# Optimization experiments

Measured on AMD Instinct MI355X. Metric: run time of the kernel, lower is better.

## Reference

```python
import jax, jax.numpy as jnp
import numpy as np

N = 20000      # nodes
E1 = 100000    # topo (2d) edges
E2 = 100000    # distance edges
HID = 128      # hidden_size
N2D = 128      # node_embed_size_2d
E2D = 64       # edge_embed_size_2d
EF = 128       # edge_feat_size
ET = 32        # edge_type_size
NRBF = 64
CUT = 6.0


def rbf_expand(d):
    # Gaussian radial basis with cosine cutoff envelope, d: [E]
    centers = jnp.linspace(0.0, CUT, NRBF)
    width = CUT / NRBF
    env = 0.5 * (jnp.cos(jnp.pi * jnp.clip(d / CUT, 0.0, 1.0)) + 1.0)
    return jnp.exp(-((d[:, None] - centers) ** 2) / (2.0 * width * width)) * env[:, None]


def setup_inputs() -> dict:
    key = jax.random.key(0)
    ks = jax.random.split(key, 20)
    s = 0.02
    return {
        "H": jax.random.normal(ks[0], (N, HID), jnp.float32),
        "V": jax.random.normal(ks[1], (N, HID, 3), jnp.float32),
        "Z": jax.random.normal(ks[2], (N, 3), jnp.float32) * 3.0,
        "layer_i": 0,
        "H_2d": jax.random.normal(ks[3], (N, N2D), jnp.float32),
        "mask_2d": jnp.ones((N,), bool),
        "E2d_idx": jax.random.randint(ks[4], (2, E1), 0, N),
        "E2d_feat": jax.random.normal(ks[5], (E2D, E1), jnp.float32),
        "Z_3d": jax.random.normal(ks[6], (N, 3), jnp.float32) * 3.0,
        "mask_3d": jnp.ones((N,), bool),
        "Edist_idx": jax.random.randint(ks[7], (2, E2), 0, N),
        "Edist_val": jax.random.uniform(ks[8], (E2,), jnp.float32) * CUT,
        "virtual_node_embed": jax.random.normal(ks[9], (1, N2D), jnp.float32),
        "edge_type_embed": jax.random.normal(ks[10], (3, ET), jnp.float32),
        "W_rbf": jax.random.normal(ks[11], (EF, NRBF), jnp.float32) * s,
        "W_e2d": jax.random.normal(ks[12], (EF, E2D), jnp.float32) * s,
        "W_i": jax.random.normal(ks[13], (HID, HID + N2D), jnp.float32) * s,
        "W_phi1": jax.random.normal(ks[14], (HID, HID + EF + ET), jnp.float32) * s,
        "b_phi1": jnp.zeros((HID,), jnp.float32),
        "W_phi2": jax.random.normal(ks[15], (3 * HID, HID), jnp.float32) * s,
        "b_phi2": jnp.zeros((3 * HID,), jnp.float32),
        "W_msg": jax.random.normal(ks[16], (3 * HID, NRBF), jnp.float32) * s,
        "b_msg": jnp.zeros((3 * HID,), jnp.float32),
    }


def reference(H, V, Z, layer_i, H_2d, mask_2d, E2d_idx, E2d_feat, Z_3d, mask_3d,
              Edist_idx, Edist_val, virtual_node_embed, edge_type_embed,
              W_rbf, W_e2d, W_i, W_phi1, b_phi1, W_phi2, b_phi2, W_msg, b_msg):
    n = H.shape[0]
    # mask_3d is all-True in this fixture => n_cond_3d == n (static shapes)
    nodes_real = jnp.concatenate([H, H_2d], axis=-1)                       # [n, h1+h2]
    virt = jnp.broadcast_to(virtual_node_embed, (n, virtual_node_embed.shape[1]))
    nodes_virt = jnp.concatenate([H, virt], axis=-1)                        # [n, h1+h2]
    nodes = jnp.concatenate([nodes_real, nodes_virt], axis=0) @ W_i.T      # [2n, h1]
    v = jnp.concatenate([V, jnp.zeros_like(V)], axis=0)                     # [2n, h1, 3]
    z = jnp.concatenate([Z, Z_3d], axis=0)                                  # [2n, 3]

    row_3d = jnp.arange(n)
    col_3d = jnp.arange(n) + n
    E3d = jnp.stack([jnp.concatenate([row_3d, col_3d]),
                     jnp.concatenate([col_3d, row_3d])], axis=0)            # [2, 2n]
    edges = jnp.concatenate([E2d_idx, E3d, Edist_idx], axis=-1)             # [2, E]
    e1, e3, e2 = E2d_idx.shape[1], E3d.shape[1], Edist_idx.shape[1]
    edge_type = jnp.concatenate([jnp.zeros((e1,), jnp.int32),
                                 jnp.ones((e3,), jnp.int32),
                                 jnp.full((e2,), 2, jnp.int32)])
    et = edge_type_embed[edge_type]                                         # [E, ET]
    attr2d = E2d_feat.T @ W_e2d.T                                           # [e1, EF]
    attr3d = jnp.zeros((e3, W_e2d.shape[0]), jnp.float32)                   # [e3, EF]
    attrd = rbf_expand(Edist_val) @ W_rbf.T                                 # [e2, EF]
    edge_attr = jnp.concatenate(
        [jnp.concatenate([attr2d, attr3d, attrd], axis=0), et], axis=-1)    # [E, EF+ET]

    # AdapterLayer: PaiNN-style equivariant message passing
    row, col = edges[0], edges[1]
    rel = z[row] - z[col]                                                   # [E, 3]
    dist = jnp.sqrt(jnp.sum(rel * rel, axis=-1) + 1e-8)                     # [E]
    unit = rel / dist[:, None]
    phi_in = jnp.concatenate([nodes[col], edge_attr], axis=-1)
    phi = jax.nn.silu(phi_in @ W_phi1.T + b_phi1) @ W_phi2.T + b_phi2       # [E, 3h]
    wd = rbf_expand(dist) @ W_msg.T + b_msg                                 # [E, 3h]
    m = phi * wd
    h = nodes.shape[1]
    s_msg, v_gate, r_gate = m[:, :h], m[:, h:2 * h], m[:, 2 * h:]
    dv = v[col] * v_gate[:, :, None] + unit[:, None, :] * r_gate[:, :, None]  # [E, h, 3]
    nn2 = nodes.shape[0]
    H_add = jax.ops.segment_sum(s_msg, row, num_segments=nn2)[:n]
    V_add = jax.ops.segment_sum(dv, row, num_segments=nn2)[:n]

    # eval-mode clamp
    H_add = jnp.clip(H_add, -100.0, 100.0)
    V_add = jnp.clip(V_add, -100.0, 100.0)

    mask_dist = jnp.zeros((n,), bool).at[Edist_idx[0]].set(True).at[Edist_idx[1]].set(True)
    update_mask = mask_2d | mask_3d | mask_dist
    H_add = jnp.where(update_mask[:, None], H_add, 0.0)
    V_add = jnp.where(update_mask[:, None, None], V_add, 0.0)
    return H_add, V_add
```

## Files before the change

kernel.cpp:

```cpp
#include <hip/hip_runtime.h>
#include <hip/hip_bf16.h>

#define NN   20000
#define E1N  100000
#define E2N  100000
#define NEFF 220000
#define TILE 64
#define NBLK ((NEFF + TILE - 1) / TILE)
#define NPAD (NBLK * TILE)
#define RBF_STEP   0.09523809523809523f
#define RBF_INV2W2 56.88888888888889f

typedef short  bf16x8 __attribute__((ext_vector_type(8)));
typedef float  f32x4  __attribute__((ext_vector_type(4)));

__device__ __forceinline__ float4 ld4(const float* p) {
    return *reinterpret_cast<const float4*>(p);
}
__device__ __forceinline__ ushort f2bf(float x) {
    __hip_bfloat16 h = __float2bfloat16(x);
    return *reinterpret_cast<ushort*>(&h);
}
__device__ __forceinline__ float bf2f(ushort u) {
    return __uint_as_float(((unsigned)u) << 16);
}
__device__ __forceinline__ float env_of(float d) {
    float x = fminf(fmaxf(d * (1.0f / 6.0f), 0.0f), 1.0f);
    return 0.5f * (__cosf(3.14159265358979f * x) + 1.0f);
}

__device__ __forceinline__ int edge_row(int eid, const int* __restrict__ E2d_idx,
                                        const int* __restrict__ Edist_idx) {
    if (eid < E1N) return E2d_idx[eid];
    if (eid < E1N + NN) return eid - E1N;
    return Edist_idx[eid - E1N - NN];
}

__global__ __launch_bounds__(256) void hist_kernel(
    const int* __restrict__ E2d_idx, const int* __restrict__ Edist_idx,
    int* __restrict__ hist) {
    int g = blockIdx.x * 256 + threadIdx.x;
    if (g < NEFF) atomicAdd(&hist[edge_row(g, E2d_idx, Edist_idx)], 1);
}

__global__ __launch_bounds__(1024) void scan_kernel(
    const int* __restrict__ hist, int* __restrict__ start, int* __restrict__ cursor) {
    __shared__ int buf[1024];
    __shared__ int carry;
    const int t = threadIdx.x;
    if (t == 0) carry = 0;
    __syncthreads();
    for (int chunk = 0; chunk < 20; ++chunk) {
        int idx = chunk * 1024 + t;
        int v = (idx < NN) ? hist[idx] : 0;
        buf[t] = v;
        __syncthreads();
        for (int off = 1; off < 1024; off <<= 1) {
            int x = (t >= off) ? buf[t - off] : 0;
            __syncthreads();
            buf[t] += x;
            __syncthreads();
        }
        int excl  = buf[t] - v;
        int cbase = carry;
        int tot   = buf[1023];
        if (idx <= NN) {
            start[idx] = cbase + excl;
            if (idx < NN) cursor[idx] = cbase + excl;
        }
        __syncthreads();
        if (t == 0) carry = cbase + tot;
        __syncthreads();
    }
}

__global__ __launch_bounds__(256) void scatter_kernel(
    const int* __restrict__ E2d_idx, const int* __restrict__ Edist_idx,
    int* __restrict__ cursor, int* __restrict__ order) {
    int g = blockIdx.x * 256 + threadIdx.x;
    if (g < NEFF) {
        int r = edge_row(g, E2d_idx, Edist_idx);
        int pos = atomicAdd(&cursor[r], 1);
        order[pos] = g;
    }
}

__global__ __launch_bounds__(64) void chunkrow_kernel(
    const int* __restrict__ order, const int* __restrict__ E2d_idx,
    const int* __restrict__ Edist_idx, int cap, int nch, int* __restrict__ chunk_r0) {
    int i = threadIdx.x;
    if (i < nch) {
        int p = i * cap;
        if (p >= NEFF) p = NEFF - 1;
        chunk_r0[i] = edge_row(order[p], E2d_idx, Edist_idx);
    }
}

__global__ __launch_bounds__(256) void meta_kernel(
    const int* __restrict__ order, const int* __restrict__ E2d_idx,
    const int* __restrict__ Edist_idx, const float* __restrict__ Edist_val,
    const float* __restrict__ Z, const float* __restrict__ Z3d,
    int4* __restrict__ metaI, float4* __restrict__ metaF,
    float4* __restrict__ payloadU) {
    int g = blockIdx.x * 256 + threadIdx.x;
    if (g >= NPAD) return;
    int eid = (g < NEFF) ? order[g] : -1;
    int row, col, ty, e2 = 0; float dval = 0.f;
    if (eid < 0)             { ty = 1; row = -1; col = 0; }
    else if (eid < E1N)      { ty = 0; row = E2d_idx[eid]; col = E2d_idx[E1N + eid]; e2 = eid; }
    else if (eid < E1N + NN) { ty = 1; int jj = eid - E1N; row = jj; col = jj + NN; }
    else { ty = 2; int g2 = eid - E1N - NN;
           row = Edist_idx[g2]; col = Edist_idx[E2N + g2]; dval = Edist_val[g2]; }
    int rs = (row < 0) ? 0 : row;
    float prx = Z[rs * 3], pry = Z[rs * 3 + 1], prz = Z[rs * 3 + 2];
    float pcx, pcy, pcz;
    if (col < NN) { pcx = Z[col * 3]; pcy = Z[col * 3 + 1]; pcz = Z[col * 3 + 2]; }
    else { int c = col - NN; pcx = Z3d[c * 3]; pcy = Z3d[c * 3 + 1]; pcz = Z3d[c * 3 + 2]; }
    float dx = prx - pcx, dy = pry - pcy, dz = prz - pcz;
    float dist = sqrtf(dx * dx + dy * dy + dz * dz + 1e-8f);
    float inv = 1.0f / dist;
    int vcol = (col < NN) ? col : -1;
    metaI[g] = make_int4(col, row, ty, e2);
    metaF[g] = make_float4(dist, dval, env_of(dist), env_of(dval));
    if (row >= 0)
        payloadU[g] = make_float4(dx * inv, dy * inv, dz * inv, __int_as_float(vcol));
}

__global__ __launch_bounds__(256) void prep_kernel(
    const float* __restrict__ W_phi1, const float* __restrict__ b_phi1,
    const float* __restrict__ W_e2d, const float* __restrict__ W_rbf,
    const float* __restrict__ W_phi2, const float* __restrict__ W_msg,
    const float* __restrict__ et, const float* __restrict__ W_i,
    ushort* __restrict__ W1c, ushort* __restrict__ W2b,
    ushort* __restrict__ Wmb, float* __restrict__ b_type,
    ushort* __restrict__ Wib) {
    int g = blockIdx.x * 256 + threadIdx.x;
    if (g < 32768) {
        int n = g >> 8, k = g & 255;
        float v;
        if (k < 128) v = W_phi1[n * 288 + k];
        else {
            int kk = k - 128;
            const float* Wsel = (kk < 64) ? W_e2d : W_rbf;
            int j = kk & 63;
            float s = 0.f;
            for (int a = 0; a < 128; ++a) s += W_phi1[n * 288 + 128 + a] * Wsel[a * 64 + j];
            v = s;
        }
        W1c[n * 256 + k] = f2bf(v);
    } else if (g < 81920) {
        int q = g - 32768; W2b[q] = f2bf(W_phi2[q]);
    } else if (g < 106496) {
        int q = g - 81920; Wmb[q] = f2bf(W_msg[q]);
    } else if (g < 106880) {
        int q = g - 106496; int ty = q >> 7, n = q & 127;
        float s = b_phi1[n];
        for (int a = 0; a < 32; ++a) s += W_phi1[n * 288 + 256 + a] * et[ty * 32 + a];
        b_type[q] = s;
    } else if (g < 139648) {
        int q = g - 106880; Wib[q] = f2bf(W_i[q]);
    }
}

__global__ __launch_bounds__(256) void featT_kernel(
    const float* __restrict__ feat, ushort* __restrict__ featTb) {
    __shared__ float tile[64][65];
    const int t = threadIdx.x;
    const int cbase = blockIdx.x * 64;
    for (int i = t; i < 64 * 64; i += 256) {
        int k = i >> 6, e = i & 63;
        tile[k][e] = (cbase + e < E1N) ? feat[(size_t)k * E1N + cbase + e] : 0.f;
    }
    __syncthreads();
    for (int i = t; i < 64 * 64; i += 256) {
        int e = i >> 6, k = i & 63;
        if (cbase + e < E1N) featTb[(size_t)(cbase + e) * 64 + k] = f2bf(tile[k][e]);
    }
}

__global__ __launch_bounds__(256, 2) void nodes_mfma_kernel(
    const float* __restrict__ H, const float* __restrict__ H2d,
    const float* __restrict__ virt, const ushort* __restrict__ Wib,
    ushort* __restrict__ nodesb) {
    __shared__ ushort A[64][264];
    __shared__ ushort WB[128][132];

    const int t = threadIdx.x;
    const int gbase = blockIdx.x * 64;

    for (int i = t; i < 64 * 64; i += 256) {
        int e = i >> 6, q = i & 63;
        int row = gbase + e;
        float4 v;
        if (q < 32)          v = ld4(H + (size_t)((row < NN) ? row : row - NN) * 128 + q * 4);
        else if (row < NN)   v = ld4(H2d + (size_t)row * 128 + (q - 32) * 4);
        else                 v = ld4(virt + (q - 32) * 4);
        ushort tmp[4] = {f2bf(v.x), f2bf(v.y), f2bf(v.z), f2bf(v.w)};
        *reinterpret_cast<uint2*>(&A[e][q * 4]) = *reinterpret_cast<const uint2*>(tmp);
    }
    for (int i = t; i < 128 * 16; i += 256) {
        int n = i >> 4, q = i & 15;
        *reinterpret_cast<uint4*>(&WB[n][q * 8]) =
            *reinterpret_cast<const uint4*>(Wib + (size_t)n * 256 + q * 8);
    }
    __syncthreads();

    const int w  = t >> 6, lane = t & 63;
    const int mh = w >> 1, nh = w & 1;
    const int lr = lane >> 4, lc = lane & 15;
    const int ar0 = mh * 32 + lc;

    f32x4 acc[2][4];
#pragma unroll
    for (int mt = 0; mt < 2; ++mt)
#pragma unroll
        for (int nt = 0; nt < 4; ++nt) acc[mt][nt] = (f32x4){0.f, 0.f, 0.f, 0.f};
#pragma unroll
    for (int ks = 0; ks < 4; ++ks) {
        bf16x8 a0 = *reinterpret_cast<const bf16x8*>(&A[ar0][ks * 32 + lr * 8]);
        bf16x8 a1 = *reinterpret_cast<const bf16x8*>(&A[ar0 + 16][ks * 32 + lr * 8]);
#pragma unroll
        for (int nt = 0; nt < 4; ++nt) {
            int n = nh * 64 + nt * 16 + lc;
            bf16x8 b = *reinterpret_cast<const bf16x8*>(&WB[n][ks * 32 + lr * 8]);
            acc[0][nt] = __builtin_amdgcn_mfma_f32_16x16x32_bf16(a0, b, acc[0][nt], 0, 0, 0);
            acc[1][nt] = __builtin_amdgcn_mfma_f32_16x16x32_bf16(a1, b, acc[1][nt], 0, 0, 0);
        }
    }
    __syncthreads();
    for (int i = t; i < 128 * 16; i += 256) {
        int n = i >> 4, q = i & 15;
        *reinterpret_cast<uint4*>(&WB[n][q * 8]) =
            *reinterpret_cast<const uint4*>(Wib + (size_t)n * 256 + 128 + q * 8);
    }
    __syncthreads();
#pragma unroll
    for (int ks = 4; ks < 8; ++ks) {
        bf16x8 a0 = *reinterpret_cast<const bf16x8*>(&A[ar0][ks * 32 + lr * 8]);
        bf16x8 a1 = *reinterpret_cast<const bf16x8*>(&A[ar0 + 16][ks * 32 + lr * 8]);
#pragma unroll
        for (int nt = 0; nt < 4; ++nt) {
            int n = nh * 64 + nt * 16 + lc;
            bf16x8 b = *reinterpret_cast<const bf16x8*>(&WB[n][(ks - 4) * 32 + lr * 8]);
            acc[0][nt] = __builtin_amdgcn_mfma_f32_16x16x32_bf16(a0, b, acc[0][nt], 0, 0, 0);
            acc[1][nt] = __builtin_amdgcn_mfma_f32_16x16x32_bf16(a1, b, acc[1][nt], 0, 0, 0);
        }
    }
#pragma unroll
    for (int mt = 0; mt < 2; ++mt)
#pragma unroll
        for (int nt = 0; nt < 4; ++nt)
#pragma unroll
            for (int r = 0; r < 4; ++r) {
                int e  = mh * 32 + mt * 16 + lr * 4 + r;
                int ch = nh * 64 + nt * 16 + lc;
                nodesb[(size_t)(gbase + e) * 128 + ch] = f2bf(acc[mt][nt][r]);
            }
}

template <int MODE>
__global__ __launch_bounds__(256, 2) void edge_kernel(
    const ushort* __restrict__ nodesb, const float* __restrict__ V,
    const float* __restrict__ Z, const float* __restrict__ Z3d,
    const int* __restrict__ E2d_idx, const float* __restrict__ E2d_feat,
    const ushort* __restrict__ featTb,
    const int* __restrict__ Edist_idx, const float* __restrict__ Edist_val,
    const ushort* __restrict__ W1c, const ushort* __restrict__ W2b,
    const ushort* __restrict__ Wmb, const float* __restrict__ b_type,
    const float* __restrict__ b_phi2, const float* __restrict__ b_msg,
    const int4* __restrict__ metaI, const float4* __restrict__ metaF,
    int p0, ushort* __restrict__ payloadM,
    float* __restrict__ Hout, float* __restrict__ Vout) {

    __shared__ ushort A1f[TILE * 264 + 256];
    __shared__ ushort WB[128][132];
    __shared__ float  s_bt[3][128];
    __shared__ int    s_row[TILE], s_col[TILE], s_ty[TILE], s_e2[TILE], s_vcol[TILE];
    __shared__ float  s_dist[TILE], s_dval[TILE], s_env[TILE], s_env2[TILE];
    __shared__ float  s_unit[TILE][3];

    ushort* hidp  = A1f;
    ushort* m_lds = A1f + 8704;

    const int t = threadIdx.x;
    const int gbase = blockIdx.x * TILE;

    if (MODE == 1) {
        if (t < TILE) {
            int4 mi = metaI[p0 + gbase + t];
            s_col[t] = mi.x; s_row[t] = mi.y; s_ty[t] = mi.z; s_e2[t] = mi.w;
        } else if (t < 2 * TILE) {
            int e = t - TILE;
            float4 mf = metaF[p0 + gbase + e];
            s_dist[e] = mf.x; s_dval[e] = mf.y; s_env[e] = mf.z; s_env2[e] = mf.w;
        }
    } else {
        if (t < TILE) {
            int gpos = gbase + t;
            int eid = (gpos < NEFF) ? gpos : -1;
            int row, col, ty, e2 = 0; float dval = 0.f;
            if (eid < 0)             { ty = 1; row = -1; col = 0; }
            else if (eid < E1N)      { ty = 0; row = E2d_idx[eid]; col = E2d_idx[E1N + eid]; e2 = eid; }
            else if (eid < E1N + NN) { ty = 1; int jj = eid - E1N; row = jj; col = jj + NN; }
            else { ty = 2; int g2 = eid - E1N - NN;
                   row = Edist_idx[g2]; col = Edist_idx[E2N + g2]; dval = Edist_val[g2]; }
            int rs = (row < 0) ? 0 : row;
            float prx = Z[rs * 3], pry = Z[rs * 3 + 1], prz = Z[rs * 3 + 2];
            float pcx, pcy, pcz;
            if (col < NN) { pcx = Z[col * 3]; pcy = Z[col * 3 + 1]; pcz = Z[col * 3 + 2]; }
            else { int c = col - NN; pcx = Z3d[c * 3]; pcy = Z3d[c * 3 + 1]; pcz = Z3d[c * 3 + 2]; }
            float dx = prx - pcx, dy = pry - pcy, dz = prz - pcz;
            float dist = sqrtf(dx * dx + dy * dy + dz * dz + 1e-8f);
            float inv = 1.0f / dist;
            s_row[t] = row; s_col[t] = col; s_ty[t] = ty; s_e2[t] = e2;
            s_vcol[t] = (col < NN) ? col : -1;
            s_unit[t][0] = dx * inv; s_unit[t][1] = dy * inv; s_unit[t][2] = dz * inv;
            s_dist[t] = dist; s_dval[t] = dval;
            s_env[t] = env_of(dist); s_env2[t] = env_of(dval);
        }
    }
    for (int i = t; i < 384; i += 256) ((float*)s_bt)[i] = b_type[i];
    __syncthreads();

    for (int i = t; i < TILE * 16; i += 256) {
        int e = i >> 4, q = i & 15;
        *reinterpret_cast<uint4*>(&A1f[e * 264 + q * 8]) =
            *reinterpret_cast<const uint4*>(nodesb + (size_t)s_col[e] * 128 + q * 8);
    }
    if (MODE == 1) {
        for (int i = t; i < TILE * 128; i += 256) {
            int e = i >> 7, k = i & 127;
            int ty = s_ty[e];
            ushort v = 0;
            if (ty == 0) { if (k < 64) v = featTb[(size_t)s_e2[e] * 64 + k]; }
            else if (ty == 2) {
                if (k >= 64) {
                    float dd = s_dval[e] - (float)(k - 64) * RBF_STEP;
                    v = f2bf(__expf(-dd * dd * RBF_INV2W2) * s_env2[e]);
                }
            }
            A1f[e * 264 + 128 + k] = v;
        }
    } else {
        for (int i = t; i < TILE * 128; i += 256) {
            int k = i >> 6, e = i & 63;
            int ty = s_ty[e];
            float v = 0.f;
            if (ty == 0) { if (k < 64) v = E2d_feat[(size_t)k * E1N + s_e2[e]]; }
            else if (ty == 2) {
                if (k >= 64) {
                    float dd = s_dval[e] - (float)(k - 64) * RBF_STEP;
                    v = __expf(-dd * dd * RBF_INV2W2) * s_env2[e];
                }
            }
            A1f[e * 264 + 128 + k] = f2bf(v);
        }
    }
    for (int i = t; i < 128 * 16; i += 256) {
        int n = i >> 4, q = i & 15;
        *reinterpret_cast<uint4*>(&WB[n][q * 8]) =
            *reinterpret_cast<const uint4*>(W1c + (size_t)n * 256 + q * 8);
    }
    __syncthreads();

    const int w  = t >> 6, lane = t & 63;
    const int mh = w >> 1, nh = w & 1;
    const int lr = lane >> 4, lc = lane & 15;
    const int ar0 = mh * 32 + lc;

    bf16x8 ra0[2], ra1[2];
    {
        float dA = s_dist[ar0],      eA = s_env[ar0];
        float dB = s_dist[ar0 + 16], eB = s_env[ar0 + 16];
#pragma unroll
        for (int ks = 0; ks < 2; ++ks)
#pragma unroll
            for (int j = 0; j < 8; ++j) {
                float c  = (float)(ks * 32 + lr * 8 + j) * RBF_STEP;
                float tA = dA - c, tB = dB - c;
                ra0[ks][j] = (short)f2bf(__expf(-tA * tA * RBF_INV2W2) * eA);
                ra1[ks][j] = (short)f2bf(__expf(-tB * tB * RBF_INV2W2) * eB);
            }
    }

    f32x4 acc[2][4];
#pragma unroll
    for (int mt = 0; mt < 2; ++mt)
#pragma unroll
        for (int nt = 0; nt < 4; ++nt) acc[mt][nt] = (f32x4){0.f, 0.f, 0.f, 0.f};
#pragma unroll
    for (int ks = 0; ks < 4; ++ks) {
        bf16x8 a0 = *reinterpret_cast<const bf16x8*>(&A1f[ar0 * 264 + ks * 32 + lr * 8]);
        bf16x8 a1 = *reinterpret_cast<const bf16x8*>(&A1f[(ar0 + 16) * 264 + ks * 32 + lr * 8]);
#pragma unroll
        for (int nt = 0; nt < 4; ++nt) {
            int n = nh * 64 + nt * 16 + lc;
            bf16x8 b = *reinterpret_cast<const bf16x8*>(&WB[n][ks * 32 + lr * 8]);
            acc[0][nt] = __builtin_amdgcn_mfma_f32_16x16x32_bf16(a0, b, acc[0][nt], 0, 0, 0);
            acc[1][nt] = __builtin_amdgcn_mfma_f32_16x16x32_bf16(a1, b, acc[1][nt], 0, 0, 0);
        }
    }
    __syncthreads();
    for (int i = t; i < 128 * 16; i += 256) {
        int n = i >> 4, q = i & 15;
        *reinterpret_cast<uint4*>(&WB[n][q * 8]) =
            *reinterpret_cast<const uint4*>(W1c + (size_t)n * 256 + 128 + q * 8);
    }
    __syncthreads();
#pragma unroll
    for (int ks = 4; ks < 8; ++ks) {
        bf16x8 a0 = *reinterpret_cast<const bf16x8*>(&A1f[ar0 * 264 + ks * 32 + lr * 8]);
        bf16x8 a1 = *reinterpret_cast<const bf16x8*>(&A1f[(ar0 + 16) * 264 + ks * 32 + lr * 8]);
#pragma unroll
        for (int nt = 0; nt < 4; ++nt) {
            int n = nh * 64 + nt * 16 + lc;
            bf16x8 b = *reinterpret_cast<const bf16x8*>(&WB[n][(ks - 4) * 32 + lr * 8]);
            acc[0][nt] = __builtin_amdgcn_mfma_f32_16x16x32_bf16(a0, b, acc[0][nt], 0, 0, 0);
            acc[1][nt] = __builtin_amdgcn_mfma_f32_16x16x32_bf16(a1, b, acc[1][nt], 0, 0, 0);
        }
    }
    __syncthreads();

#pragma unroll
    for (int mt = 0; mt < 2; ++mt)
#pragma unroll
        for (int nt = 0; nt < 4; ++nt)
#pragma unroll
            for (int r = 0; r < 4; ++r) {
                int e  = mh * 32 + mt * 16 + lr * 4 + r;
                int ch = nh * 64 + nt * 16 + lc;
                float x = acc[mt][nt][r] + s_bt[s_ty[e]][ch];
                hidp[e * 136 + ch] = f2bf(x / (1.0f + __expf(-x)));
            }
    for (int i = t; i < 128 * 16; i += 256) {
        int n = i >> 4, q = i & 15;
        *reinterpret_cast<uint4*>(&WB[n][q * 8]) =
            *reinterpret_cast<const uint4*>(W2b + (size_t)n * 128 + q * 8);
    }
    __syncthreads();

    bf16x8 ha0[4], ha1[4];
#pragma unroll
    for (int ks = 0; ks < 4; ++ks) {
        ha0[ks] = *reinterpret_cast<const bf16x8*>(&hidp[ar0 * 136 + ks * 32 + lr * 8]);
        ha1[ks] = *reinterpret_cast<const bf16x8*>(&hidp[(ar0 + 16) * 136 + ks * 32 + lr * 8]);
    }

    f32x4 vgr[2][4];
#pragma unroll
    for (int c = 0; c < 3; ++c) {
        f32x4 p[2][4], g[2][4];
#pragma unroll
        for (int mt = 0; mt < 2; ++mt)
#pragma unroll
            for (int nt = 0; nt < 4; ++nt) {
                p[mt][nt] = (f32x4){0.f, 0.f, 0.f, 0.f};
                g[mt][nt] = (f32x4){0.f, 0.f, 0.f, 0.f};
            }
#pragma unroll
        for (int ks = 0; ks < 4; ++ks) {
#pragma unroll
            for (int nt = 0; nt < 4; ++nt) {
                int n = nh * 64 + nt * 16 + lc;
                bf16x8 b = *reinterpret_cast<const bf16x8*>(&WB[n][ks * 32 + lr * 8]);
                p[0][nt] = __builtin_amdgcn_mfma_f32_16x16x32_bf16(ha0[ks], b, p[0][nt], 0, 0, 0);
                p[1][nt] = __builtin_amdgcn_mfma_f32_16x16x32_bf16(ha1[ks], b, p[1][nt], 0, 0, 0);
            }
        }
#pragma unroll
        for (int ks = 0; ks < 2; ++ks) {
#pragma unroll
            for (int nt = 0; nt < 4; ++nt) {
                int n = c * 128 + nh * 64 + nt * 16 + lc;
                bf16x8 b = *reinterpret_cast<const bf16x8*>(Wmb + (size_t)n * 64 + ks * 32 + lr * 8);
                g[0][nt] = __builtin_amdgcn_mfma_f32_16x16x32_bf16(ra0[ks], b, g[0][nt], 0, 0, 0);
                g[1][nt] = __builtin_amdgcn_mfma_f32_16x16x32_bf16(ra1[ks], b, g[1][nt], 0, 0, 0);
            }
        }
        __syncthreads();
        if (c < 2) {
            for (int i = t; i < 128 * 16; i += 256) {
                int n = i >> 4, q = i & 15;
                *reinterpret_cast<uint4*>(&WB[n][q * 8]) =
                    *reinterpret_cast<const uint4*>(W2b + (size_t)((c + 1) * 128 + n) * 128 + q * 8);
            }
        }
#pragma unroll
        for (int mt = 0; mt < 2; ++mt)
#pragma unroll
            for (int nt = 0; nt < 4; ++nt) {
                int d  = nh * 64 + nt * 16 + lc;
                float b2 = b_phi2[c * 128 + d];
                float bm = b_msg[c * 128 + d];
#pragma unroll
                for (int r = 0; r < 4; ++r) {
                    int e = mh * 32 + mt * 16 + lr * 4 + r;
                    float m = (p[mt][nt][r] + b2) * (g[mt][nt][r] + bm);
                    if (MODE == 1) {
                        m_lds[e * 132 + d] = f2bf(m);
                    } else {
                        int row = s_row[e];
                        if (c == 0) {
                            if (row >= 0) unsafeAtomicAdd(&Hout[(size_t)row * 128 + d], m);
                        } else if (c == 1) {
                            vgr[mt][nt][r] = m;
                        } else if (row >= 0) {
                            float vgv = vgr[mt][nt][r];
                            int vc = s_vcol[e];
                            float vx = 0.f, vy = 0.f, vz = 0.f;
                            if (vc >= 0) {
                                const float* vp = V + ((size_t)vc * 128 + d) * 3;
                                vx = vp[0]; vy = vp[1]; vz = vp[2];
                            }
                            float* vo = Vout + ((size_t)row * 128 + d) * 3;
                            unsafeAtomicAdd(vo + 0, vx * vgv + s_unit[e][0] * m);
                            unsafeAtomicAdd(vo + 1, vy * vgv + s_unit[e][1] * m);
                            unsafeAtomicAdd(vo + 2, vz * vgv + s_unit[e][2] * m);
                        }
                    }
                }
            }
        __syncthreads();
        if (MODE == 1) {
            for (int i = t; i < 2048; i += 256) {
                int e = i >> 5, q = i & 31;
                *reinterpret_cast<uint2*>(payloadM + (size_t)(gbase + e) * 384 + c * 128 + q * 4) =
                    *reinterpret_cast<const uint2*>(m_lds + e * 132 + q * 4);
            }
        }
    }
}

__global__ __launch_bounds__(256) void reduce_kernel(
    const ushort* __restrict__ payloadM, const float4* __restrict__ payloadU,
    const float* __restrict__ V, const int* __restrict__ start,
    const int* __restrict__ chunk_r0, int ci, int p0, int p1,
    float* __restrict__ Hout, float* __restrict__ Vout) {
    const int t = threadIdx.x;
    const int rbase = chunk_r0[ci] + blockIdx.x * 8;
    const bool hside = (t < 128);
    const int d = hside ? t : (t - 128);
    for (int nr = 0; nr < 8; ++nr) {
        int r = rbase + nr;
        if (r >= NN) return;
        int s0 = start[r], s1 = start[r + 1];
        if (s0 >= p1) return;
        int a = (s0 > p0) ? s0 : p0;
        int b = (s1 < p1) ? s1 : p1;
        if (a >= b) continue;
        int n = b - a;
        if (hside) {
            const ushort* base = payloadM + (size_t)(a - p0) * 384 + d;
            float a0 = 0.f, a1 = 0.f, a2 = 0.f, a3 = 0.f;
            int i = 0;
            for (; i + 4 <= n; i += 4) {
                a0 += bf2f(base[(size_t)i * 384]);
                a1 += bf2f(base[(size_t)(i + 1) * 384]);
                a2 += bf2f(base[(size_t)(i + 2) * 384]);
                a3 += bf2f(base[(size_t)(i + 3) * 384]);
            }
            for (; i < n; ++i) a0 += bf2f(base[(size_t)i * 384]);
            float acc = (a0 + a1) + (a2 + a3);
            float* ptr = &Hout[(size_t)r * 128 + d];
            float o = *ptr + acc;
            if (s1 <= p1) o = fminf(fmaxf(o, -100.f), 100.f);
            *ptr = o;
        } else {
            const ushort* base = payloadM + (size_t)(a - p0) * 384;
            const float4* ub = payloadU + a;
            float ax = 0.f, ay = 0.f, az = 0.f;
            float bx = 0.f, by = 0.f, bz = 0.f;
            int i = 0;
            for (; i + 2 <= n; i += 2) {
                const ushort* pm0 = base + (size_t)i * 384;
                const ushort* pm1 = base + (size_t)(i + 1) * 384;
                float vg0 = bf2f(pm0[128 + d]), rg0 = bf2f(pm0[256 + d]);
                float vg1 = bf2f(pm1[128 + d]), rg1 = bf2f(pm1[256 + d]);
                float4 u0 = ub[i];
                float4 u1 = ub[i + 1];
                int vc0 = __float_as_int(u0.w);
                int vc1 = __float_as_int(u1.w);
                if (vc0 >= 0) {
                    const float* vp = V + (size_t)vc0 * 384 + d * 3;
                    ax += vg0 * vp[0]; ay += vg0 * vp[1]; az += vg0 * vp[2];
                }
                if (vc1 >= 0) {
                    const float* vp = V + (size_t)vc1 * 384 + d * 3;
                    bx += vg1 * vp[0]; by += vg1 * vp[1]; bz += vg1 * vp[2];
                }
                ax += rg0 * u0.x; ay += rg0 * u0.y; az += rg0 * u0.z;
                bx += rg1 * u1.x; by += rg1 * u1.y; bz += rg1 * u1.z;
            }
            if (i < n) {
                const ushort* pm0 = base + (size_t)i * 384;
                float vg0 = bf2f(pm0[128 + d]), rg0 = bf2f(pm0[256 + d]);
                float4 u0 = ub[i];
                int vc0 = __float_as_int(u0.w);
                if (vc0 >= 0) {
                    const float* vp = V + (size_t)vc0 * 384 + d * 3;
                    ax += vg0 * vp[0]; ay += vg0 * vp[1]; az += vg0 * vp[2];
                }
                ax += rg0 * u0.x; ay += rg0 * u0.y; az += rg0 * u0.z;
            }
            ax += bx; ay += by; az += bz;
            float* vo = Vout + (size_t)r * 384 + d * 3;
            float ox = vo[0] + ax, oy = vo[1] + ay, oz = vo[2] + az;
            if (s1 <= p1) {
                ox = fminf(fmaxf(ox, -100.f), 100.f);
                oy = fminf(fmaxf(oy, -100.f), 100.f);
                oz = fminf(fmaxf(oz, -100.f), 100.f);
            }
            vo[0] = ox; vo[1] = oy; vo[2] = oz;
        }
    }
}

extern "C" void kernel_launch(void* const* d_in, const int* in_sizes, int n_in,
                              void* d_out, int out_size, void* d_ws, size_t ws_size,
                              hipStream_t stream) {
    const float* H         = (const float*)d_in[0];
    const float* V         = (const float*)d_in[1];
    const float* Z         = (const float*)d_in[2];
    const float* H2d       = (const float*)d_in[4];
    const int*   E2d_idx   = (const int*)d_in[6];
    const float* E2d_feat  = (const float*)d_in[7];
    const float* Z3d       = (const float*)d_in[8];
    const int*   Edist_idx = (const int*)d_in[10];
    const float* Edist_val = (const float*)d_in[11];
    const float* virt      = (const float*)d_in[12];
    const float* et        = (const float*)d_in[13];
    const float* W_rbf     = (const float*)d_in[14];
    const float* W_e2d     = (const float*)d_in[15];
    const float* W_i       = (const float*)d_in[16];
    const float* W_phi1    = (const float*)d_in[17];
    const float* b_phi1    = (const float*)d_in[18];
    const float* W_phi2    = (const float*)d_in[19];
    const float* b_phi2    = (const float*)d_in[20];
    const float* W_msg     = (const float*)d_in[21];
    const float* b_msg     = (const float*)d_in[22];

    ushort* nodesb  = (ushort*)d_ws;
    ushort* W1c     = nodesb + 5120000;
    ushort* W2b     = W1c + 32768;
    ushort* Wmb     = W2b + 49152;
    ushort* Wib     = Wmb + 24576;
    float*  b_type  = (float*)(Wib + 32768);
    ushort* featTb  = (ushort*)(b_type + 384);
    int*    hist    = (int*)(featTb + (size_t)E1N * 64);
    int*    cursor  = hist + NN;
    int*    start   = cursor + NN;
    int*    order   = start + NN + 1;
    int*    chunk_r0= order + NPAD;
    int4*   metaI   = (int4*)(((size_t)(chunk_r0 + 64) + 15) & ~(size_t)15);
    float4* metaF   = (float4*)(metaI + NPAD);
    float4* payloadU= metaF + NPAD;

    size_t fixed = (size_t)((char*)(payloadU + NPAD) - (char*)d_ws);
    size_t poff  = (fixed + 255) & ~(size_t)255;
    size_t avail = (ws_size > poff) ? (ws_size - poff) : 0;
    long long cap_ll = (long long)(avail / 768) / TILE * TILE;
    int cap = (cap_ll > (long long)NPAD) ? NPAD : (int)cap_ll;
    const bool big = (cap >= 4096);
    ushort* payloadM = (ushort*)((char*)d_ws + poff);

    float* Hout = (float*)d_out;
    float* Vout = Hout + (size_t)NN * 128;

    hipMemsetAsync(d_out, 0, (size_t)out_size * sizeof(float), stream);
    prep_kernel<<<(139648 + 255) / 256, 256, 0, stream>>>(
        W_phi1, b_phi1, W_e2d, W_rbf, W_phi2, W_msg, et, W_i,
        W1c, W2b, Wmb, b_type, Wib);
    nodes_mfma_kernel<<<(2 * NN) / 64, 256, 0, stream>>>(H, H2d, virt, Wib, nodesb);

    if (big) {
        hipMemsetAsync(hist, 0, NN * sizeof(int), stream);
        featT_kernel<<<(E1N + 63) / 64, 256, 0, stream>>>(E2d_feat, featTb);
        hist_kernel<<<(NEFF + 255) / 256, 256, 0, stream>>>(E2d_idx, Edist_idx, hist);
        scan_kernel<<<1, 1024, 0, stream>>>(hist, start, cursor);
        scatter_kernel<<<(NEFF + 255) / 256, 256, 0, stream>>>(E2d_idx, Edist_idx, cursor, order);
        meta_kernel<<<(NPAD + 255) / 256, 256, 0, stream>>>(
            order, E2d_idx, Edist_idx, Edist_val, Z, Z3d, metaI, metaF, payloadU);
        int bpc = cap / TILE;
        int nch = (NBLK + bpc - 1) / bpc;
        chunkrow_kernel<<<1, 64, 0, stream>>>(order, E2d_idx, Edist_idx, cap, nch, chunk_r0);
        int rbound = (NN < cap + 1) ? NN : (cap + 1);
        int rgrid  = (rbound + 7) / 8;
        for (int ci = 0; ci < nch; ++ci) {
            int b0 = ci * bpc;
            int nb = ((NBLK - b0) < bpc) ? (NBLK - b0) : bpc;
            int p0 = b0 * TILE;
            int p1 = p0 + nb * TILE; if (p1 > NEFF) p1 = NEFF;
            edge_kernel<1><<<nb, 256, 0, stream>>>(
                nodesb, V, Z, Z3d, E2d_idx, E2d_feat, featTb, Edist_idx, Edist_val,
                W1c, W2b, Wmb, b_type, b_phi2, b_msg, metaI, metaF, p0, payloadM,
                Hout, Vout);
            reduce_kernel<<<rgrid, 256, 0, stream>>>(payloadM, payloadU, V, start,
                                                     chunk_r0, ci, p0, p1, Hout, Vout);
        }
    } else {
        edge_kernel<0><<<NBLK, 256, 0, stream>>>(
            nodesb, V, Z, Z3d, E2d_idx, E2d_feat, featTb, Edist_idx, Edist_val,
            W1c, W2b, Wmb, b_type, b_phi2, b_msg, metaI, metaF, 0, payloadM,
            Hout, Vout);
    }
}
```

Measured before the change: 405.2 us.

## Single-pass edge kernel with register A-operands and unchunked CSR reduce

Replaces the chunked edge/reduce loop with one edge kernel over all edges followed by one reduce pass, provided the workspace can hold the whole bf16 message payload. The reduce now writes clipped results directly, so the output memset, the chunk-row kernel and the read-modify-write of outputs are all dropped. The new edge kernel builds its A operands in registers straight from global memory instead of staging them in LDS, which shrinks shared memory enough to allow 3 blocks per CU. The scan is rewritten as a 256-thread serial-plus-shuffle scan. The trade-offs are a large workspace requirement and possibly higher register pressure at the new occupancy target.

Result: slower. 443.7 us (+9.5%).

```diff
diff --git a/kernel.cpp b/kernel.cpp
--- a/kernel.cpp
+++ b/kernel.cpp
@@ -28,6 +28,9 @@
     float x = fminf(fmaxf(d * (1.0f / 6.0f), 0.0f), 1.0f);
     return 0.5f * (__cosf(3.14159265358979f * x) + 1.0f);
 }
+__device__ __forceinline__ float clip100(float x) {
+    return fminf(fmaxf(x, -100.f), 100.f);
+}
 
 __device__ __forceinline__ int edge_row(int eid, const int* __restrict__ E2d_idx,
                                         const int* __restrict__ Edist_idx) {
@@ -43,35 +46,36 @@
     if (g < NEFF) atomicAdd(&hist[edge_row(g, E2d_idx, Edist_idx)], 1);
 }
 
-__global__ __launch_bounds__(1024) void scan_kernel(
+__global__ __launch_bounds__(256) void scan_kernel(
     const int* __restrict__ hist, int* __restrict__ start, int* __restrict__ cursor) {
-    __shared__ int buf[1024];
-    __shared__ int carry;
+    __shared__ int wsum[4];
     const int t = threadIdx.x;
-    if (t == 0) carry = 0;
-    __syncthreads();
-    for (int chunk = 0; chunk < 20; ++chunk) {
-        int idx = chunk * 1024 + t;
-        int v = (idx < NN) ? hist[idx] : 0;
-        buf[t] = v;
-        __syncthreads();
-        for (int off = 1; off < 1024; off <<= 1) {
-            int x = (t >= off) ? buf[t - off] : 0;
-            __syncthreads();
-            buf[t] += x;
-            __syncthreads();
-        }
-        int excl  = buf[t] - v;
-        int cbase = carry;
-        int tot   = buf[1023];
-        if (idx <= NN) {
-            start[idx] = cbase + excl;
-            if (idx < NN) cursor[idx] = cbase + excl;
-        }
-        __syncthreads();
-        if (t == 0) carry = cbase + tot;
-        __syncthreads();
-    }
+    const int base = t * 80;
+    int s = 0;
+    for (int j = 0; j < 80; ++j) {
+        int idx = base + j;
+        if (idx < NN) s += hist[idx];
+    }
+    const int lane = t & 63, w = t >> 6;
+    int v = s;
+    for (int off = 1; off < 64; off <<= 1) {
+        int x = __shfl_up(v, off, 64);
+        if (lane >= off) v += x;
+    }
+    if (lane == 63) wsum[w] = v;
+    __syncthreads();
+    int woff = 0;
+    for (int i = 0; i < w; ++i) woff += wsum[i];
+    int run = woff + v - s;
+    for (int j = 0; j < 80; ++j) {
+        int idx = base + j;
+        if (idx < NN) {
+            start[idx] = run;
+            cursor[idx] = run;
+            run += hist[idx];
+        }
+    }
+    if (t == 255) start[NN] = run;
 }
 
 __global__ __launch_bounds__(256) void scatter_kernel(
@@ -85,23 +89,12 @@
     }
 }
 
-__global__ __launch_bounds__(64) void chunkrow_kernel(
-    const int* __restrict__ order, const int* __restrict__ E2d_idx,
-    const int* __restrict__ Edist_idx, int cap, int nch, int* __restrict__ chunk_r0) {
-    int i = threadIdx.x;
-    if (i < nch) {
-        int p = i * cap;
-        if (p >= NEFF) p = NEFF - 1;
-        chunk_r0[i] = edge_row(order[p], E2d_idx, Edist_idx);
-    }
-}
-
 __global__ __launch_bounds__(256) void meta_kernel(
     const int* __restrict__ order, const int* __restrict__ E2d_idx,
     const int* __restrict__ Edist_idx, const float* __restrict__ Edist_val,
     const float* __restrict__ Z, const float* __restrict__ Z3d,
     int4* __restrict__ metaI, float4* __restrict__ metaF,
-    float4* __restrict__ payloadU) {
+    float4* __restrict__ metaU) {
     int g = blockIdx.x * 256 + threadIdx.x;
     if (g >= NPAD) return;
     int eid = (g < NEFF) ? order[g] : -1;
@@ -122,8 +115,9 @@
     int vcol = (col < NN) ? col : -1;
     metaI[g] = make_int4(col, row, ty, e2);
     metaF[g] = make_float4(dist, dval, env_of(dist), env_of(dval));
-    if (row >= 0)
-        payloadU[g] = make_float4(dx * inv, dy * inv, dz * inv, __int_as_float(vcol));
+    metaU[g] = (row >= 0)
+        ? make_float4(dx * inv, dy * inv, dz * inv, __int_as_float(vcol))
+        : make_float4(0.f, 0.f, 0.f, __int_as_float(-1));
 }
 
 __global__ __launch_bounds__(256) void prep_kernel(
@@ -258,108 +252,266 @@
             }
 }
 
-template <int MODE>
-__global__ __launch_bounds__(256, 2) void edge_kernel(
+__global__ __launch_bounds__(256, 3) void edge1_kernel(
+    const ushort* __restrict__ nodesb, const ushort* __restrict__ featTb,
+    const ushort* __restrict__ W1c, const ushort* __restrict__ W2b,
+    const ushort* __restrict__ Wmb, const float* __restrict__ b_type,
+    const float* __restrict__ b_phi2, const float* __restrict__ b_msg,
+    const int4* __restrict__ metaI, const float4* __restrict__ metaF,
+    ushort* __restrict__ payloadM) {
+
+    __shared__ ushort sm[26752];
+    ushort* WB   = sm;
+    ushort* HM   = sm + 16896;
+    float*  s_bt = (float*)(sm + 25600);
+    int*    s_col= (int*)(sm + 26368);
+    int*    s_ty = (int*)(sm + 26496);
+    int*    s_e2 = (int*)(sm + 26624);
+
+    const int t = threadIdx.x;
+    const int gbase = blockIdx.x * TILE;
+
+    if (t < TILE) {
+        int4 mi = metaI[gbase + t];
+        s_col[t] = mi.x; s_ty[t] = mi.z; s_e2[t] = mi.w;
+    }
+    for (int i = t; i < 384; i += 256) s_bt[i] = b_type[i];
+    for (int i = t; i < 128 * 16; i += 256) {
+        int n = i >> 4, q = i & 15;
+        *reinterpret_cast<uint4*>(WB + n * 132 + q * 8) =
+            *reinterpret_cast<const uint4*>(W1c + (size_t)n * 256 + q * 8);
+    }
+    __syncthreads();
+
+    const int w  = t >> 6, lane = t & 63;
+    const int mh = w >> 1, nh = w & 1;
+    const int lr = lane >> 4, lc = lane & 15;
+    const int ar0 = mh * 32 + lc;
+
+    const int colA = s_col[ar0],      colB = s_col[ar0 + 16];
+    const int tyA  = s_ty[ar0],       tyB  = s_ty[ar0 + 16];
+    const int e2A  = s_e2[ar0],       e2B  = s_e2[ar0 + 16];
+    const float4 mfA = metaF[gbase + ar0];
+    const float4 mfB = metaF[gbase + ar0 + 16];
+
+    bf16x8 a0[8], a1[8];
+    const bf16x8 zz = {0, 0, 0, 0, 0, 0, 0, 0};
+#pragma unroll
+    for (int ks = 0; ks < 4; ++ks) {
+        a0[ks] = *reinterpret_cast<const bf16x8*>(nodesb + (size_t)colA * 128 + ks * 32 + lr * 8);
+        a1[ks] = *reinterpret_cast<const bf16x8*>(nodesb + (size_t)colB * 128 + ks * 32 + lr * 8);
+    }
+#pragma unroll
+    for (int ks = 4; ks < 6; ++ks) {
+        bf16x8 fA = *reinterpret_cast<const bf16x8*>(featTb + (size_t)e2A * 64 + (ks - 4) * 32 + lr * 8);
+        bf16x8 fB = *reinterpret_cast<const bf16x8*>(featTb + (size_t)e2B * 64 + (ks - 4) * 32 + lr * 8);
+        a0[ks] = (tyA == 0) ? fA : zz;
+        a1[ks] = (tyB == 0) ? fB : zz;
+    }
+#pragma unroll
+    for (int ks = 6; ks < 8; ++ks) {
+#pragma unroll
+        for (int j = 0; j < 8; ++j) {
+            float cc = (float)((ks - 6) * 32 + lr * 8 + j) * RBF_STEP;
+            float tA = mfA.y - cc, tB = mfB.y - cc;
+            ushort vA = f2bf(__expf(-tA * tA * RBF_INV2W2) * mfA.w);
+            ushort vB = f2bf(__expf(-tB * tB * RBF_INV2W2) * mfB.w);
+            a0[ks][j] = (tyA == 2) ? (short)vA : (short)0;
+            a1[ks][j] = (tyB == 2) ? (short)vB : (short)0;
+        }
+    }
+    bf16x8 ra0[2], ra1[2];
+#pragma unroll
+    for (int ks = 0; ks < 2; ++ks)
+#pragma unroll
+        for (int j = 0; j < 8; ++j) {
+            float cc = (float)(ks * 32 + lr * 8 + j) * RBF_STEP;
+            float tA = mfA.x - cc, tB = mfB.x - cc;
+            ra0[ks][j] = (short)f2bf(__expf(-tA * tA * RBF_INV2W2) * mfA.z);
+            ra1[ks][j] = (short)f2bf(__expf(-tB * tB * RBF_INV2W2) * mfB.z);
+        }
+
+    f32x4 acc[2][4];
+#pragma unroll
+    for (int mt = 0; mt < 2; ++mt)
+#pragma unroll
+        for (int nt = 0; nt < 4; ++nt) acc[mt][nt] = (f32x4){0.f, 0.f, 0.f, 0.f};
+#pragma unroll
+    for (int ks = 0; ks < 4; ++ks) {
+#pragma unroll
+        for (int nt = 0; nt < 4; ++nt) {
+            int n = nh * 64 + nt * 16 + lc;
+            bf16x8 b = *reinterpret_cast<const bf16x8*>(WB + n * 132 + ks * 32 + lr * 8);
+            acc[0][nt] = __builtin_amdgcn_mfma_f32_16x16x32_bf16(a0[ks], b, acc[0][nt], 0, 0, 0);
+            acc[1][nt] = __builtin_amdgcn_mfma_f32_16x16x32_bf16(a1[ks], b, acc[1][nt], 0, 0, 0);
+        }
+    }
+    __syncthreads();
+    for (int i = t; i < 128 * 16; i += 256) {
+        int n = i >> 4, q = i & 15;
+        *reinterpret_cast<uint4*>(WB + n * 132 + q * 8) =
+            *reinterpret_cast<const uint4*>(W1c + (size_t)n * 256 + 128 + q * 8);
+    }
+    __syncthreads();
+#pragma unroll
+    for (int ks = 4; ks < 8; ++ks) {
+#pragma unroll
+        for (int nt = 0; nt < 4; ++nt) {
+            int n = nh * 64 + nt * 16 + lc;
+            bf16x8 b = *reinterpret_cast<const bf16x8*>(WB + n * 132 + (ks - 4) * 32 + lr * 8);
+            acc[0][nt] = __builtin_amdgcn_mfma_f32_16x16x32_bf16(a0[ks], b, acc[0][nt], 0, 0, 0);
+            acc[1][nt] = __builtin_amdgcn_mfma_f32_16x16x32_bf16(a1[ks], b, acc[1][nt], 0, 0, 0);
+        }
+    }
+    __syncthreads();
+
+#pragma unroll
+    for (int mt = 0; mt < 2; ++mt)
+#pragma unroll
+        for (int nt = 0; nt < 4; ++nt)
+#pragma unroll
+            for (int r = 0; r < 4; ++r) {
+                int e  = mh * 32 + mt * 16 + lr * 4 + r;
+                int ch = nh * 64 + nt * 16 + lc;
+                float x = acc[mt][nt][r] + s_bt[s_ty[e] * 128 + ch];
+                HM[e * 136 + ch] = f2bf(x / (1.0f + __expf(-x)));
+            }
+    for (int i = t; i < 128 * 16; i += 256) {
+        int n = i >> 4, q = i & 15;
+        *reinterpret_cast<uint4*>(WB + n * 132 + q * 8) =
+            *reinterpret_cast<const uint4*>(W2b + (size_t)n * 128 + q * 8);
+    }
+    __syncthreads();
+
+    bf16x8 ha0[4], ha1[4];
+#pragma unroll
+    for (int ks = 0; ks < 4; ++ks) {
+        ha0[ks] = *reinterpret_cast<const bf16x8*>(HM + ar0 * 136 + ks * 32 + lr * 8);
+        ha1[ks] = *reinterpret_cast<const bf16x8*>(HM + (ar0 + 16) * 136 + ks * 32 + lr * 8);
+    }
+
+#pragma unroll
+    for (int c = 0; c < 3; ++c) {
+        f32x4 p[2][4], g[2][4];
+#pragma unroll
+        for (int mt = 0; mt < 2; ++mt)
+#pragma unroll
+            for (int nt = 0; nt < 4; ++nt) {
+                p[mt][nt] = (f32x4){0.f, 0.f, 0.f, 0.f};
+                g[mt][nt] = (f32x4){0.f, 0.f, 0.f, 0.f};
+            }
+#pragma unroll
+        for (int ks = 0; ks < 4; ++ks) {
+#pragma unroll
+            for (int nt = 0; nt < 4; ++nt) {
+                int n = nh * 64 + nt * 16 + lc;
+                bf16x8 b = *reinterpret_cast<const bf16x8*>(WB + n * 132 + ks * 32 + lr * 8);
+                p[0][nt] = __builtin_amdgcn_mfma_f32_16x16x32_bf16(ha0[ks], b, p[0][nt], 0, 0, 0);
+                p[1][nt] = __builtin_amdgcn_mfma_f32_16x16x32_bf16(ha1[ks], b, p[1][nt], 0, 0, 0);
+            }
+        }
+#pragma unroll
+        for (int ks = 0; ks < 2; ++ks) {
+#pragma unroll
+            for (int nt = 0; nt < 4; ++nt) {
+                int n = c * 128 + nh * 64 + nt * 16 + lc;
+                bf16x8 b = *reinterpret_cast<const bf16x8*>(Wmb + (size_t)n * 64 + ks * 32 + lr * 8);
+                g[0][nt] = __builtin_amdgcn_mfma_f32_16x16x32_bf16(ra0[ks], b, g[0][nt], 0, 0, 0);
+                g[1][nt] = __builtin_amdgcn_mfma_f32_16x16x32_bf16(ra1[ks], b, g[1][nt], 0, 0, 0);
+            }
+        }
+        __syncthreads();
+#pragma unroll
+        for (int mt = 0; mt < 2; ++mt)
+#pragma unroll
+            for (int nt = 0; nt < 4; ++nt) {
+                int d  = nh * 64 + nt * 16 + lc;
+                float b2 = b_phi2[c * 128 + d];
+                float bm = b_msg[c * 128 + d];
+#pragma unroll
+                for (int r = 0; r < 4; ++r) {
+                    int e = mh * 32 + mt * 16 + lr * 4 + r;
+                    HM[e * 136 + d] = f2bf((p[mt][nt][r] + b2) * (g[mt][nt][r] + bm));
+                }
+            }
+        if (c < 2) {
+            for (int i = t; i < 128 * 16; i += 256) {
+                int n = i >> 4, q = i & 15;
+                *reinterpret_cast<uint4*>(WB + n * 132 + q * 8) =
+                    *reinterpret_cast<const uint4*>(W2b + (size_t)((c + 1) * 128 + n) * 128 + q * 8);
+            }
+        }
+        __syncthreads();
+        for (int i = t; i < 2048; i += 256) {
+            int e = i >> 5, q = i & 31;
+            *reinterpret_cast<uint2*>(payloadM + (size_t)(gbase + e) * 384 + c * 128 + q * 4) =
+                *reinterpret_cast<const uint2*>(HM + e * 136 + q * 4);
+        }
+    }
+}
+
+__global__ __launch_bounds__(256, 2) void edge0_kernel(
     const ushort* __restrict__ nodesb, const float* __restrict__ V,
     const float* __restrict__ Z, const float* __restrict__ Z3d,
     const int* __restrict__ E2d_idx, const float* __restrict__ E2d_feat,
-    const ushort* __restrict__ featTb,
     const int* __restrict__ Edist_idx, const float* __restrict__ Edist_val,
     const ushort* __restrict__ W1c, const ushort* __restrict__ W2b,
     const ushort* __restrict__ Wmb, const float* __restrict__ b_type,
     const float* __restrict__ b_phi2, const float* __restrict__ b_msg,
-    const int4* __restrict__ metaI, const float4* __restrict__ metaF,
-    int p0, ushort* __restrict__ payloadM,
     float* __restrict__ Hout, float* __restrict__ Vout) {
 
-    __shared__ ushort A1f[TILE * 264 + 256];
-    __shared__ ushort WB[128][132];
+    __shared__ ushort A1[TILE][264];
     __shared__ float  s_bt[3][128];
     __shared__ int    s_row[TILE], s_col[TILE], s_ty[TILE], s_e2[TILE], s_vcol[TILE];
     __shared__ float  s_dist[TILE], s_dval[TILE], s_env[TILE], s_env2[TILE];
     __shared__ float  s_unit[TILE][3];
-
-    ushort* hidp  = A1f;
-    ushort* m_lds = A1f + 8704;
+    ushort (*hid)[136] = reinterpret_cast<ushort(*)[136]>(&A1[0][0]);
 
     const int t = threadIdx.x;
     const int gbase = blockIdx.x * TILE;
-
-    if (MODE == 1) {
-        if (t < TILE) {
-            int4 mi = metaI[p0 + gbase + t];
-            s_col[t] = mi.x; s_row[t] = mi.y; s_ty[t] = mi.z; s_e2[t] = mi.w;
-        } else if (t < 2 * TILE) {
-            int e = t - TILE;
-            float4 mf = metaF[p0 + gbase + e];
-            s_dist[e] = mf.x; s_dval[e] = mf.y; s_env[e] = mf.z; s_env2[e] = mf.w;
-        }
-    } else {
-        if (t < TILE) {
-            int gpos = gbase + t;
-            int eid = (gpos < NEFF) ? gpos : -1;
-            int row, col, ty, e2 = 0; float dval = 0.f;
-            if (eid < 0)             { ty = 1; row = -1; col = 0; }
-            else if (eid < E1N)      { ty = 0; row = E2d_idx[eid]; col = E2d_idx[E1N + eid]; e2 = eid; }
-            else if (eid < E1N + NN) { ty = 1; int jj = eid - E1N; row = jj; col = jj + NN; }
-            else { ty = 2; int g2 = eid - E1N - NN;
-                   row = Edist_idx[g2]; col = Edist_idx[E2N + g2]; dval = Edist_val[g2]; }
-            int rs = (row < 0) ? 0 : row;
-            float prx = Z[rs * 3], pry = Z[rs * 3 + 1], prz = Z[rs * 3 + 2];
-            float pcx, pcy, pcz;
-            if (col < NN) { pcx = Z[col * 3]; pcy = Z[col * 3 + 1]; pcz = Z[col * 3 + 2]; }
-            else { int c = col - NN; pcx = Z3d[c * 3]; pcy = Z3d[c * 3 + 1]; pcz = Z3d[c * 3 + 2]; }
-            float dx = prx - pcx, dy = pry - pcy, dz = prz - pcz;
-            float dist = sqrtf(dx * dx + dy * dy + dz * dz + 1e-8f);
-            float inv = 1.0f / dist;
-            s_row[t] = row; s_col[t] = col; s_ty[t] = ty; s_e2[t] = e2;
-            s_vcol[t] = (col < NN) ? col : -1;
-            s_unit[t][0] = dx * inv; s_unit[t][1] = dy * inv; s_unit[t][2] = dz * inv;
-            s_dist[t] = dist; s_dval[t] = dval;
-            s_env[t] = env_of(dist); s_env2[t] = env_of(dval);
-        }
+    if (t < TILE) {
+        int gpos = gbase + t;
+        int eid = (gpos < NEFF) ? gpos : -1;
+        int row, col, ty, e2 = 0; float dval = 0.f;
+        if (eid < 0)             { ty = 1; row = -1; col = 0; }
+        else if (eid < E1N)      { ty = 0; row = E2d_idx[eid]; col = E2d_idx[E1N + eid]; e2 = eid; }
+        else if (eid < E1N + NN) { ty = 1; int jj = eid - E1N; row = jj; col = jj + NN; }
+        else { ty = 2; int g2 = eid - E1N - NN;
+               row = Edist_idx[g2]; col = Edist_idx[E2N + g2]; dval = Edist_val[g2]; }
+        int rs = (row < 0) ? 0 : row;
+        float prx = Z[rs * 3], pry = Z[rs * 3 + 1], prz = Z[rs * 3 + 2];
+        float pcx, pcy, pcz;
+        if (col < NN) { pcx = Z[col * 3]; pcy = Z[col * 3 + 1]; pcz = Z[col * 3 + 2]; }
+        else { int c = col - NN; pcx = Z3d[c * 3]; pcy = Z3d[c * 3 + 1]; pcz = Z3d[c * 3 + 2]; }
+        float dx = prx - pcx, dy = pry - pcy, dz = prz - pcz;
+        float dist = sqrtf(dx * dx + dy * dy + dz * dz + 1e-8f);
+        float inv = 1.0f / dist;
+        s_row[t] = row; s_col[t] = col; s_ty[t] = ty; s_e2[t] = e2;
+        s_vcol[t] = (col < NN) ? col : -1;
+        s_unit[t][0] = dx * inv; s_unit[t][1] = dy * inv; s_unit[t][2] = dz * inv;
+        s_dist[t] = dist; s_dval[t] = dval;
+        s_env[t] = env_of(dist); s_env2[t] = env_of(dval);
     }
     for (int i = t; i < 384; i += 256) ((float*)s_bt)[i] = b_type[i];
     __syncthreads();
 
     for (int i = t; i < TILE * 16; i += 256) {
         int e = i >> 4, q = i & 15;
-        *reinterpret_cast<uint4*>(&A1f[e * 264 + q * 8]) =
+        *reinterpret_cast<uint4*>(&A1[e][q * 8]) =
             *reinterpret_cast<const uint4*>(nodesb + (size_t)s_col[e] * 128 + q * 8);
     }
-    if (MODE == 1) {
-        for (int i = t; i < TILE * 128; i += 256) {
-            int e = i >> 7, k = i & 127;
-            int ty = s_ty[e];
-            ushort v = 0;
-            if (ty == 0) { if (k < 64) v = featTb[(size_t)s_e2[e] * 64 + k]; }
-            else if (ty == 2) {
-                if (k >= 64) {
-                    float dd = s_dval[e] - (float)(k - 64) * RBF_STEP;
-                    v = f2bf(__expf(-dd * dd * RBF_INV2W2) * s_env2[e]);
-                }
-            }
-            A1f[e * 264 + 128 + k] = v;
-        }
-    } else {
-        for (int i = t; i < TILE * 128; i += 256) {
-            int k = i >> 6, e = i & 63;
-            int ty = s_ty[e];
-            float v = 0.f;
-            if (ty == 0) { if (k < 64) v = E2d_feat[(size_t)k * E1N + s_e2[e]]; }
-            else if (ty == 2) {
-                if (k >= 64) {
-                    float dd = s_dval[e] - (float)(k - 64) * RBF_STEP;
-                    v = __expf(-dd * dd * RBF_INV2W2) * s_env2[e];
-                }
-            }
-            A1f[e * 264 + 128 + k] = f2bf(v);
-        }
-    }
-    for (int i = t; i < 128 * 16; i += 256) {
-        int n = i >> 4, q = i & 15;
-        *reinterpret_cast<uint4*>(&WB[n][q * 8]) =
-            *reinterpret_cast<const uint4*>(W1c + (size_t)n * 256 + q * 8);
+    for (int i = t; i < TILE * 128; i += 256) {
+        int k = i >> 6, e = i & 63;
+        int ty = s_ty[e];
+        float v = 0.f;
+        if (ty == 0) { if (k < 64) v = E2d_feat[(size_t)k * E1N + s_e2[e]]; }
+        else if (ty == 2) {
+            if (k >= 64) {
+                float dd = s_dval[e] - (float)(k - 64) * RBF_STEP;
+                v = __expf(-dd * dd * RBF_INV2W2) * s_env2[e];
+            }
+        }
+        A1[e][128 + k] = f2bf(v);
     }
     __syncthreads();
 
@@ -389,38 +541,18 @@
 #pragma unroll
         for (int nt = 0; nt < 4; ++nt) acc[mt][nt] = (f32x4){0.f, 0.f, 0.f, 0.f};
 #pragma unroll
-    for (int ks = 0; ks < 4; ++ks) {
-        bf16x8 a0 = *reinterpret_cast<const bf16x8*>(&A1f[ar0 * 264 + ks * 32 + lr * 8]);
-        bf16x8 a1 = *reinterpret_cast<const bf16x8*>(&A1f[(ar0 + 16) * 264 + ks * 32 + lr * 8]);
+    for (int ks = 0; ks < 8; ++ks) {
+        bf16x8 a0 = *reinterpret_cast<const bf16x8*>(&A1[ar0][ks * 32 + lr * 8]);
+        bf16x8 a1 = *reinterpret_cast<const bf16x8*>(&A1[ar0 + 16][ks * 32 + lr * 8]);
 #pragma unroll
         for (int nt = 0; nt < 4; ++nt) {
             int n = nh * 64 + nt * 16 + lc;
-            bf16x8 b = *reinterpret_cast<const bf16x8*>(&WB[n][ks * 32 + lr * 8]);
+            bf16x8 b = *reinterpret_cast<const bf16x8*>(W1c + (size_t)n * 256 + ks * 32 + lr * 8);
             acc[0][nt] = __builtin_amdgcn_mfma_f32_16x16x32_bf16(a0, b, acc[0][nt], 0, 0, 0);
             acc[1][nt] = __builtin_amdgcn_mfma_f32_16x16x32_bf16(a1, b, acc[1][nt], 0, 0, 0);
         }
     }
     __syncthreads();
-    for (int i = t; i < 128 * 16; i += 256) {
-        int n = i >> 4, q = i & 15;
-        *reinterpret_cast<uint4*>(&WB[n][q * 8]) =
-            *reinterpret_cast<const uint4*>(W1c + (size_t)n * 256 + 128 + q * 8);
-    }
-    __syncthreads();
-#pragma unroll
-    for (int ks = 4; ks < 8; ++ks) {
-        bf16x8 a0 = *reinterpret_cast<const bf16x8*>(&A1f[ar0 * 264 + ks * 32 + lr * 8]);
-        bf16x8 a1 = *reinterpret_cast<const bf16x8*>(&A1f[(ar0 + 16) * 264 + ks * 32 + lr * 8]);
-#pragma unroll
-        for (int nt = 0; nt < 4; ++nt) {
-            int n = nh * 64 + nt * 16 + lc;
-            bf16x8 b = *reinterpret_cast<const bf16x8*>(&WB[n][(ks - 4) * 32 + lr * 8]);
-            acc[0][nt] = __builtin_amdgcn_mfma_f32_16x16x32_bf16(a0, b, acc[0][nt], 0, 0, 0);
-            acc[1][nt] = __builtin_amdgcn_mfma_f32_16x16x32_bf16(a1, b, acc[1][nt], 0, 0, 0);
-        }
-    }
-    __syncthreads();
-
 #pragma unroll
     for (int mt = 0; mt < 2; ++mt)
 #pragma unroll
@@ -430,21 +562,9 @@
                 int e  = mh * 32 + mt * 16 + lr * 4 + r;
                 int ch = nh * 64 + nt * 16 + lc;
                 float x = acc[mt][nt][r] + s_bt[s_ty[e]][ch];
-                hidp[e * 136 + ch] = f2bf(x / (1.0f + __expf(-x)));
-            }
-    for (int i = t; i < 128 * 16; i += 256) {
-        int n = i >> 4, q = i & 15;
-        *reinterpret_cast<uint4*>(&WB[n][q * 8]) =
-            *reinterpret_cast<const uint4*>(W2b + (size_t)n * 128 + q * 8);
-    }
-    __syncthreads();
-
-    bf16x8 ha0[4], ha1[4];
-#pragma unroll
-    for (int ks = 0; ks < 4; ++ks) {
-        ha0[ks] = *reinterpret_cast<const bf16x8*>(&hidp[ar0 * 136 + ks * 32 + lr * 8]);
-        ha1[ks] = *reinterpret_cast<const bf16x8*>(&hidp[(ar0 + 16) * 136 + ks * 32 + lr * 8]);
-    }
+                hid[e][ch] = f2bf(x / (1.0f + __expf(-x)));
+            }
+    __syncthreads();
 
     f32x4 vgr[2][4];
 #pragma unroll
@@ -459,12 +579,14 @@
             }
 #pragma unroll
         for (int ks = 0; ks < 4; ++ks) {
+            bf16x8 a0 = *reinterpret_cast<const bf16x8*>(&hid[ar0][ks * 32 + lr * 8]);
+            bf16x8 a1 = *reinterpret_cast<const bf16x8*>(&hid[ar0 + 16][ks * 32 + lr * 8]);
 #pragma unroll
             for (int nt = 0; nt < 4; ++nt) {
-                int n = nh * 64 + nt * 16 + lc;
-                bf16x8 b = *reinterpret_cast<const bf16x8*>(&WB[n][ks * 32 + lr * 8]);
-                p[0][nt] = __builtin_amdgcn_mfma_f32_16x16x32_bf16(ha0[ks], b, p[0][nt], 0, 0, 0);
-                p[1][nt] = __builtin_amdgcn_mfma_f32_16x16x32_bf16(ha1[ks], b, p[1][nt], 0, 0, 0);
+                int n = c * 128 + nh * 64 + nt * 16 + lc;
+                bf16x8 b = *reinterpret_cast<const bf16x8*>(W2b + (size_t)n * 128 + ks * 32 + lr * 8);
+                p[0][nt] = __builtin_amdgcn_mfma_f32_16x16x32_bf16(a0, b, p[0][nt], 0, 0, 0);
+                p[1][nt] = __builtin_amdgcn_mfma_f32_16x16x32_bf16(a1, b, p[1][nt], 0, 0, 0);
             }
         }
 #pragma unroll
@@ -477,14 +599,6 @@
                 g[1][nt] = __builtin_amdgcn_mfma_f32_16x16x32_bf16(ra1[ks], b, g[1][nt], 0, 0, 0);
             }
         }
-        __syncthreads();
-        if (c < 2) {
-            for (int i = t; i < 128 * 16; i += 256) {
-                int n = i >> 4, q = i & 15;
-                *reinterpret_cast<uint4*>(&WB[n][q * 8]) =
-                    *reinterpret_cast<const uint4*>(W2b + (size_t)((c + 1) * 128 + n) * 128 + q * 8);
-            }
-        }
 #pragma unroll
         for (int mt = 0; mt < 2; ++mt)
 #pragma unroll
@@ -496,61 +610,44 @@
                 for (int r = 0; r < 4; ++r) {
                     int e = mh * 32 + mt * 16 + lr * 4 + r;
                     float m = (p[mt][nt][r] + b2) * (g[mt][nt][r] + bm);
-                    if (MODE == 1) {
-                        m_lds[e * 132 + d] = f2bf(m);
-                    } else {
-                        int row = s_row[e];
-                        if (c == 0) {
-                            if (row >= 0) unsafeAtomicAdd(&Hout[(size_t)row * 128 + d], m);
-                        } else if (c == 1) {
-                            vgr[mt][nt][r] = m;
-                        } else if (row >= 0) {
-                            float vgv = vgr[mt][nt][r];
-                            int vc = s_vcol[e];
-                            float vx = 0.f, vy = 0.f, vz = 0.f;
-                            if (vc >= 0) {
-                                const float* vp = V + ((size_t)vc * 128 + d) * 3;
-                                vx = vp[0]; vy = vp[1]; vz = vp[2];
-                            }
-                            float* vo = Vout + ((size_t)row * 128 + d) * 3;
-                            unsafeAtomicAdd(vo + 0, vx * vgv + s_unit[e][0] * m);
-                            unsafeAtomicAdd(vo + 1, vy * vgv + s_unit[e][1] * m);
-                            unsafeAtomicAdd(vo + 2, vz * vgv + s_unit[e][2] * m);
+                    int row = s_row[e];
+                    if (c == 0) {
+                        if (row >= 0) unsafeAtomicAdd(&Hout[(size_t)row * 128 + d], m);
+                    } else if (c == 1) {
+                        vgr[mt][nt][r] = m;
+                    } else if (row >= 0) {
+                        float vgv = vgr[mt][nt][r];
+                        int vc = s_vcol[e];
+                        float vx = 0.f, vy = 0.f, vz = 0.f;
+                        if (vc >= 0) {
+                            const float* vp = V + ((size_t)vc * 128 + d) * 3;
+                            vx = vp[0]; vy = vp[1]; vz = vp[2];
                         }
+                        float* vo = Vout + ((size_t)row * 128 + d) * 3;
+                        unsafeAtomicAdd(vo + 0, vx * vgv + s_unit[e][0] * m);
+                        unsafeAtomicAdd(vo + 1, vy * vgv + s_unit[e][1] * m);
+                        unsafeAtomicAdd(vo + 2, vz * vgv + s_unit[e][2] * m);
                     }
                 }
             }
-        __syncthreads();
-        if (MODE == 1) {
-            for (int i = t; i < 2048; i += 256) {
-                int e = i >> 5, q = i & 31;
-                *reinterpret_cast<uint2*>(payloadM + (size_t)(gbase + e) * 384 + c * 128 + q * 4) =
-                    *reinterpret_cast<const uint2*>(m_lds + e * 132 + q * 4);
-            }
-        }
     }
 }
 
 __global__ __launch_bounds__(256) void reduce_kernel(
-    const ushort* __restrict__ payloadM, const float4* __restrict__ payloadU,
+    const ushort* __restrict__ payloadM, const float4* __restrict__ metaU,
     const float* __restrict__ V, const int* __restrict__ start,
-    const int* __restrict__ chunk_r0, int ci, int p0, int p1,
     float* __restrict__ Hout, float* __restrict__ Vout) {
     const int t = threadIdx.x;
-    const int rbase = chunk_r0[ci] + blockIdx.x * 8;
+    const int rbase = blockIdx.x * 8;
     const bool hside = (t < 128);
     const int d = hside ? t : (t - 128);
     for (int nr = 0; nr < 8; ++nr) {
         int r = rbase + nr;
         if (r >= NN) return;
-        int s0 = start[r], s1 = start[r + 1];
-        if (s0 >= p1) return;
-        int a = (s0 > p0) ? s0 : p0;
-        int b = (s1 < p1) ? s1 : p1;
-        if (a >= b) continue;
+        int a = start[r], b = start[r + 1];
         int n = b - a;
         if (hside) {
-            const ushort* base = payloadM + (size_t)(a - p0) * 384 + d;
+            const ushort* base = payloadM + (size_t)a * 384 + d;
             float a0 = 0.f, a1 = 0.f, a2 = 0.f, a3 = 0.f;
             int i = 0;
             for (; i + 4 <= n; i += 4) {
@@ -560,14 +657,10 @@
                 a3 += bf2f(base[(size_t)(i + 3) * 384]);
             }
             for (; i < n; ++i) a0 += bf2f(base[(size_t)i * 384]);
-            float acc = (a0 + a1) + (a2 + a3);
-            float* ptr = &Hout[(size_t)r * 128 + d];
-            float o = *ptr + acc;
-            if (s1 <= p1) o = fminf(fmaxf(o, -100.f), 100.f);
-            *ptr = o;
+            Hout[(size_t)r * 128 + d] = clip100((a0 + a1) + (a2 + a3));
         } else {
-            const ushort* base = payloadM + (size_t)(a - p0) * 384;
-            const float4* ub = payloadU + a;
+            const ushort* base = payloadM + (size_t)a * 384;
+            const float4* ub = metaU + a;
             float ax = 0.f, ay = 0.f, az = 0.f;
             float bx = 0.f, by = 0.f, bz = 0.f;
             int i = 0;
@@ -602,15 +695,10 @@
                 }
                 ax += rg0 * u0.x; ay += rg0 * u0.y; az += rg0 * u0.z;
             }
-            ax += bx; ay += by; az += bz;
             float* vo = Vout + (size_t)r * 384 + d * 3;
-            float ox = vo[0] + ax, oy = vo[1] + ay, oz = vo[2] + az;
-            if (s1 <= p1) {
-                ox = fminf(fmaxf(ox, -100.f), 100.f);
-                oy = fminf(fmaxf(oy, -100.f), 100.f);
-                oz = fminf(fmaxf(oz, -100.f), 100.f);
-            }
-            vo[0] = ox; vo[1] = oy; vo[2] = oz;
+            vo[0] = clip100(ax + bx);
+            vo[1] = clip100(ay + by);
+            vo[2] = clip100(az + bz);
         }
     }
 }
@@ -650,23 +738,19 @@
     int*    cursor  = hist + NN;
     int*    start   = cursor + NN;
     int*    order   = start + NN + 1;
-    int*    chunk_r0= order + NPAD;
-    int4*   metaI   = (int4*)(((size_t)(chunk_r0 + 64) + 15) & ~(size_t)15);
+    int4*   metaI   = (int4*)(((size_t)(order + NPAD) + 15) & ~(size_t)15);
     float4* metaF   = (float4*)(metaI + NPAD);
-    float4* payloadU= metaF + NPAD;
-
-    size_t fixed = (size_t)((char*)(payloadU + NPAD) - (char*)d_ws);
+    float4* metaU   = metaF + NPAD;
+
+    size_t fixed = (size_t)((char*)(metaU + NPAD) - (char*)d_ws);
     size_t poff  = (fixed + 255) & ~(size_t)255;
-    size_t avail = (ws_size > poff) ? (ws_size - poff) : 0;
-    long long cap_ll = (long long)(avail / 768) / TILE * TILE;
-    int cap = (cap_ll > (long long)NPAD) ? NPAD : (int)cap_ll;
-    const bool big = (cap >= 4096);
+    size_t need  = poff + (size_t)NPAD * 384 * sizeof(ushort);
+    const bool big = (ws_size >= need);
     ushort* payloadM = (ushort*)((char*)d_ws + poff);
 
     float* Hout = (float*)d_out;
     float* Vout = Hout + (size_t)NN * 128;
 
-    hipMemsetAsync(d_out, 0, (size_t)out_size * sizeof(float), stream);
     prep_kernel<<<(139648 + 255) / 256, 256, 0, stream>>>(
         W_phi1, b_phi1, W_e2d, W_rbf, W_phi2, W_msg, et, W_i,
         W1c, W2b, Wmb, b_type, Wib);
@@ -676,31 +760,19 @@
         hipMemsetAsync(hist, 0, NN * sizeof(int), stream);
         featT_kernel<<<(E1N + 63) / 64, 256, 0, stream>>>(E2d_feat, featTb);
         hist_kernel<<<(NEFF + 255) / 256, 256, 0, stream>>>(E2d_idx, Edist_idx, hist);
-        scan_kernel<<<1, 1024, 0, stream>>>(hist, start, cursor);
+        scan_kernel<<<1, 256, 0, stream>>>(hist, start, cursor);
         scatter_kernel<<<(NEFF + 255) / 256, 256, 0, stream>>>(E2d_idx, Edist_idx, cursor, order);
         meta_kernel<<<(NPAD + 255) / 256, 256, 0, stream>>>(
-            order, E2d_idx, Edist_idx, Edist_val, Z, Z3d, metaI, metaF, payloadU);
-        int bpc = cap / TILE;
-        int nch = (NBLK + bpc - 1) / bpc;
-        chunkrow_kernel<<<1, 64, 0, stream>>>(order, E2d_idx, Edist_idx, cap, nch, chunk_r0);
-        int rbound = (NN < cap + 1) ? NN : (cap + 1);
-        int rgrid  = (rbound + 7) / 8;
-        for (int ci = 0; ci < nch; ++ci) {
-            int b0 = ci * bpc;
-            int nb = ((NBLK - b0) < bpc) ? (NBLK - b0) : bpc;
-            int p0 = b0 * TILE;
-            int p1 = p0 + nb * TILE; if (p1 > NEFF) p1 = NEFF;
-            edge_kernel<1><<<nb, 256, 0, stream>>>(
-                nodesb, V, Z, Z3d, E2d_idx, E2d_feat, featTb, Edist_idx, Edist_val,
-                W1c, W2b, Wmb, b_type, b_phi2, b_msg, metaI, metaF, p0, payloadM,
-                Hout, Vout);
-            reduce_kernel<<<rgrid, 256, 0, stream>>>(payloadM, payloadU, V, start,
-                                                     chunk_r0, ci, p0, p1, Hout, Vout);
-        }
+            order, E2d_idx, Edist_idx, Edist_val, Z, Z3d, metaI, metaF, metaU);
+        edge1_kernel<<<NBLK, 256, 0, stream>>>(
+            nodesb, featTb, W1c, W2b, Wmb, b_type, b_phi2, b_msg,
+            metaI, metaF, payloadM);
+        reduce_kernel<<<(NN + 7) / 8, 256, 0, stream>>>(
+            payloadM, metaU, V, start, Hout, Vout);
     } else {
-        edge_kernel<0><<<NBLK, 256, 0, stream>>>(
-            nodesb, V, Z, Z3d, E2d_idx, E2d_feat, featTb, Edist_idx, Edist_val,
-            W1c, W2b, Wmb, b_type, b_phi2, b_msg, metaI, metaF, 0, payloadM,
-            Hout, Vout);
-    }
-}
+        hipMemsetAsync(d_out, 0, (size_t)out_size * sizeof(float), stream);
+        edge0_kernel<<<NBLK, 256, 0, stream>>>(
+            nodesb, V, Z, Z3d, E2d_idx, E2d_feat, Edist_idx, Edist_val,
+            W1c, W2b, Wmb, b_type, b_phi2, b_msg, Hout, Vout);
+    }
+}
```
